# Kernel optimization log

Hardware: AMD Instinct MI355X
Metric: run time of the kernel (lower is better)

## Reference

```python
import jax, jax.numpy as jnp
import numpy as np

T, B, IN_DIM, D_VALUE, D_KEY = 1024, 8, 512, 64, 64
EPS = 1e-8

def setup_inputs() -> dict:
    key = jax.random.key(0)
    ks = jax.random.split(key, 7)
    s = 1.0 / np.sqrt(IN_DIM)
    return {
        "x":  jax.random.normal(ks[0], (T, B, IN_DIM), dtype=jnp.float32),
        "Wv": jax.random.uniform(ks[1], (D_VALUE, IN_DIM), jnp.float32, -s, s),
        "bv": jax.random.uniform(ks[2], (D_VALUE,), jnp.float32, -s, s),
        "Wk": jax.random.uniform(ks[3], (D_KEY, IN_DIM), jnp.float32, -s, s),
        "bk": jax.random.uniform(ks[4], (D_KEY,), jnp.float32, -s, s),
        "Wa": jax.random.uniform(ks[5], (D_KEY, IN_DIM), jnp.float32, -s, s),
        "ba": jax.random.uniform(ks[6], (D_KEY,), jnp.float32, -s, s),
    }

def reference(x, Wv, bv, Wk, bk, Wa, ba):
    # Projections: x (T,B,in_dim) -> v (T,B,d), k (T,B,n), alpha (T,B,n)
    v = jnp.einsum('tbi,di->tbd', x, Wv) + bv
    k = jnp.einsum('tbi,ni->tbn', x, Wk) + bk
    alpha = jax.nn.sigmoid(jnp.einsum('tbi,ni->tbn', x, Wa) + ba)
    # outer product per timestep: (T,B,d,n)
    outer = jnp.einsum('tbd,tbn->tbdn', v, k)
    # log-space cumulative decay, normalized by final cumprod
    log_cumprod = jnp.cumsum(jnp.log(jnp.maximum(alpha, EPS)), axis=0)  # (T,B,n)
    cumprod = jnp.exp(log_cumprod)
    decay = cumprod / (cumprod[-1:] + EPS)
    weighted = outer * decay[:, :, None, :]  # (T,B,d,n)
    S = jnp.cumsum(weighted, axis=0)
    return S
```

## Files before the change

### kernel.cpp

```cpp
#include <hip/hip_runtime.h>
#include <math.h>

#define T_DIM  1024
#define B_DIM  8
#define IN_D   512
#define NROWS  (T_DIM * B_DIM)
#define EPSF   1e-8f

#define CHUNK  16
#define NCHUNK (T_DIM / CHUNK)
#define SEG    16
#define NSEG   (T_DIM / SEG)

typedef float vfloat4 __attribute__((ext_vector_type(4)));

#define OFF_WT   0
#define OFF_V    (OFF_WT + IN_D * 192)
#define OFF_K    (OFF_V  + NROWS * 64)
#define OFF_Z    (OFF_K  + NROWS * 64)
#define OFF_SEG  (OFF_Z  + NROWS * 64)
#define OFF_TOT  (OFF_SEG + NSEG * B_DIM * 64)
#define OFF_P    (OFF_TOT + B_DIM * 64)

__global__ void k0_wt(const float* __restrict__ Wv, const float* __restrict__ Wk,
                      const float* __restrict__ Wa, float* __restrict__ Wt) {
    int idx = blockIdx.x * 256 + threadIdx.x;
    int i = idx / 192, c = idx % 192;
    float v;
    if (c < 64)       v = Wv[c * IN_D + i];
    else if (c < 128) v = Wk[(c - 64) * IN_D + i];
    else              v = Wa[(c - 128) * IN_D + i];
    Wt[i * 192 + c] = v;
}

__global__ __launch_bounds__(256) void k1_proj(
        const float* __restrict__ x, const float* __restrict__ Wt,
        const float* __restrict__ bv, const float* __restrict__ bk, const float* __restrict__ ba,
        float* __restrict__ V, float* __restrict__ Kb, float* __restrict__ Zb) {
    __shared__ float xs[2][32][32];
    __shared__ float wsm[2][32][192];
    const int tid  = threadIdx.x;
    const int h    = tid >> 7;
    const int t7   = tid & 127;
    const int rq   = t7 >> 4;
    const int cq   = t7 & 15;
    const int row0 = blockIdx.x * 32;

    float4 acc[4][3];
#pragma unroll
    for (int j = 0; j < 4; ++j)
#pragma unroll
        for (int m = 0; m < 3; ++m) acc[j][m] = make_float4(0.f, 0.f, 0.f, 0.f);

    for (int s = 0; s < 8; ++s) {
#pragma unroll
        for (int q = 0; q < 2; ++q) {
            int idx = tid + q * 256;
            int hh = idx >> 8, r = idx & 31, f = (idx >> 5) & 7;
            float4 v4 = reinterpret_cast<const float4*>(x)[((row0 + r) * IN_D + hh * 256 + s * 32 + f * 4) >> 2];
            xs[hh][f * 4 + 0][r] = v4.x;
            xs[hh][f * 4 + 1][r] = v4.y;
            xs[hh][f * 4 + 2][r] = v4.z;
            xs[hh][f * 4 + 3][r] = v4.w;
        }
#pragma unroll
        for (int q = 0; q < 12; ++q) {
            int idx = tid + q * 256;
            int hh = idx / 1536;
            int rem = idx - hh * 1536;
            int kk = rem / 48;
            int f  = rem - kk * 48;
            float4 v4 = reinterpret_cast<const float4*>(Wt)[((hh * 256 + s * 32 + kk) * 192 + f * 4) >> 2];
            *reinterpret_cast<float4*>(&wsm[hh][kk][f * 4]) = v4;
        }
        __syncthreads();

#pragma unroll 4
        for (int kk = 0; kk < 32; ++kk) {
            float4 xv = *reinterpret_cast<const float4*>(&xs[h][kk][rq * 4]);
#pragma unroll
            for (int m = 0; m < 3; ++m) {
                float4 wq = *reinterpret_cast<const float4*>(&wsm[h][kk][m * 64 + cq * 4]);
#pragma unroll
                for (int j = 0; j < 4; ++j) {
                    float xx = (&xv.x)[j];
                    acc[j][m].x = fmaf(xx, wq.x, acc[j][m].x);
                    acc[j][m].y = fmaf(xx, wq.y, acc[j][m].y);
                    acc[j][m].z = fmaf(xx, wq.z, acc[j][m].z);
                    acc[j][m].w = fmaf(xx, wq.w, acc[j][m].w);
                }
            }
        }
        __syncthreads();
    }

    float* red = &wsm[0][0][0];
    if (h == 1) {
#pragma unroll
        for (int j = 0; j < 4; ++j)
#pragma unroll
            for (int m = 0; m < 3; ++m)
                *reinterpret_cast<float4*>(&red[t7 * 52 + (j * 3 + m) * 4]) = acc[j][m];
    }
    __syncthreads();
    if (h == 0) {
        float4 bv4 = *reinterpret_cast<const float4*>(&bv[cq * 4]);
        float4 bk4 = *reinterpret_cast<const float4*>(&bk[cq * 4]);
        float4 ba4 = *reinterpret_cast<const float4*>(&ba[cq * 4]);
#pragma unroll
        for (int j = 0; j < 4; ++j) {
            int row = row0 + rq * 4 + j;
#pragma unroll
            for (int m = 0; m < 3; ++m) {
                float4 o = *reinterpret_cast<const float4*>(&red[t7 * 52 + (j * 3 + m) * 4]);
                o.x += (&acc[j][m].x)[0];
                o.x = acc[j][m].x + (&o.x)[0] - acc[j][m].x;
            }
            float4 o0 = *reinterpret_cast<const float4*>(&red[t7 * 52 + (j * 3 + 0) * 4]);
            float4 o1 = *reinterpret_cast<const float4*>(&red[t7 * 52 + (j * 3 + 1) * 4]);
            float4 o2 = *reinterpret_cast<const float4*>(&red[t7 * 52 + (j * 3 + 2) * 4]);
            float4 r0, r1, r2;
            r0.x = acc[j][0].x + o0.x + bv4.x; r0.y = acc[j][0].y + o0.y + bv4.y;
            r0.z = acc[j][0].z + o0.z + bv4.z; r0.w = acc[j][0].w + o0.w + bv4.w;
            r1.x = acc[j][1].x + o1.x + bk4.x; r1.y = acc[j][1].y + o1.y + bk4.y;
            r1.z = acc[j][1].z + o1.z + bk4.z; r1.w = acc[j][1].w + o1.w + bk4.w;
            r2.x = acc[j][2].x + o2.x + ba4.x; r2.y = acc[j][2].y + o2.y + ba4.y;
            r2.z = acc[j][2].z + o2.z + ba4.z; r2.w = acc[j][2].w + o2.w + ba4.w;
            *reinterpret_cast<float4*>(&V [row * 64 + cq * 4]) = r0;
            *reinterpret_cast<float4*>(&Kb[row * 64 + cq * 4]) = r1;
            *reinterpret_cast<float4*>(&Zb[row * 64 + cq * 4]) = r2;
        }
    }
}

__global__ void k2a_logs(float* __restrict__ Z, float* __restrict__ seg) {
    int b = blockIdx.x & 7, s = blockIdx.x >> 3;
    int n = threadIdx.x;
    int base = b * 64 + n;
    float accv = 0.f;
#pragma unroll
    for (int i = 0; i < SEG; ++i) {
        int t = s * SEG + i;
        float z = Z[t * 512 + base];
        float a = 1.f / (1.f + expf(-z));
        float l = logf(fmaxf(a, EPSF));
        Z[t * 512 + base] = l;
        accv += l;
    }
    seg[s * 512 + base] = accv;
}

__global__ void k2b_scan(float* __restrict__ seg, float* __restrict__ tot) {
    int i = threadIdx.x;
    float vals[NSEG];
#pragma unroll
    for (int s = 0; s < NSEG; ++s) vals[s] = seg[s * 512 + i];
    float run = 0.f;
#pragma unroll
    for (int s = 0; s < NSEG; ++s) { seg[s * 512 + i] = run; run += vals[s]; }
    tot[i] = run;
}

__global__ void k2c_w(const float* __restrict__ Z, const float* __restrict__ seg,
                      const float* __restrict__ tot, float* __restrict__ Kb) {
    int b = blockIdx.x & 7, s = blockIdx.x >> 3;
    int n = threadIdx.x;
    int base = b * 64 + n;
    float run = seg[s * 512 + base];
    float invden = 1.f / (expf(tot[base]) + EPSF);
#pragma unroll
    for (int i = 0; i < SEG; ++i) {
        int t = s * SEG + i;
        run += Z[t * 512 + base];
        Kb[t * 512 + base] *= expf(run) * invden;
    }
}

__global__ __launch_bounds__(256) void k3_partial(const float* __restrict__ V,
                                                  const float* __restrict__ W,
                                                  float* __restrict__ P) {
    __shared__ float vs[CHUNK * 64];
    __shared__ float wsh[CHUNK * 64];
    int b = blockIdx.x & 7, cch = blockIdx.x >> 3;
    int tid = threadIdx.x;
    int dg = tid >> 4, n4 = tid & 15;
    {
        int il = tid >> 4, f = tid & 15;
        int row = (cch * CHUNK + il) * 8 + b;
        reinterpret_cast<float4*>(vs)[il * 16 + f]  = reinterpret_cast<const float4*>(V)[row * 16 + f];
        reinterpret_cast<float4*>(wsh)[il * 16 + f] = reinterpret_cast<const float4*>(W)[row * 16 + f];
    }
    __syncthreads();
    float4 acc[4];
#pragma unroll
    for (int q = 0; q < 4; ++q) acc[q] = make_float4(0.f, 0.f, 0.f, 0.f);

#pragma unroll
    for (int i = 0; i < CHUNK; ++i) {
        float4 wv = reinterpret_cast<const float4*>(wsh)[i * 16 + n4];
#pragma unroll
        for (int q = 0; q < 4; ++q) {
            float vd = vs[i * 64 + dg + 16 * q];
            acc[q].x = fmaf(vd, wv.x, acc[q].x);
            acc[q].y = fmaf(vd, wv.y, acc[q].y);
            acc[q].z = fmaf(vd, wv.z, acc[q].z);
            acc[q].w = fmaf(vd, wv.w, acc[q].w);
        }
    }
    float* Pp = P + (cch * 8 + b) * 4096;
#pragma unroll
    for (int q = 0; q < 4; ++q)
        *reinterpret_cast<float4*>(Pp + (dg + 16 * q) * 64 + 4 * n4) = acc[q];
}

__global__ __launch_bounds__(256) void k4_prefix(float* __restrict__ P) {
    int gid = blockIdx.x * 256 + threadIdx.x;
    int b = gid >> 12, dn = gid & 4095;
    float run = 0.f;
#pragma unroll
    for (int c = 0; c < NCHUNK; ++c) {
        float v = P[(c * 8 + b) * 4096 + dn];
        P[(c * 8 + b) * 4096 + dn] = run;
        run += v;
    }
}

__global__ __launch_bounds__(256) void k5_main(const float* __restrict__ V,
                                               const float* __restrict__ W,
                                               const float* __restrict__ P,
                                               float* __restrict__ S) {
    __shared__ float vs[CHUNK * 64];
    __shared__ float wsh[CHUNK * 64];
    int b = blockIdx.x & 7, cch = blockIdx.x >> 3;
    int tid = threadIdx.x;
    int dg = tid >> 4, n4 = tid & 15;
    {
        int il = tid >> 4, f = tid & 15;
        int row = (cch * CHUNK + il) * 8 + b;
        reinterpret_cast<float4*>(vs)[il * 16 + f]  = reinterpret_cast<const float4*>(V)[row * 16 + f];
        reinterpret_cast<float4*>(wsh)[il * 16 + f] = reinterpret_cast<const float4*>(W)[row * 16 + f];
    }
    vfloat4 acc[4];
    const float* Pp = P + (cch * 8 + b) * 4096;
#pragma unroll
    for (int q = 0; q < 4; ++q)
        acc[q] = *reinterpret_cast<const vfloat4*>(Pp + (dg + 16 * q) * 64 + 4 * n4);
    __syncthreads();

#pragma unroll
    for (int i = 0; i < CHUNK; ++i) {
        float4 wv = reinterpret_cast<const float4*>(wsh)[i * 16 + n4];
        int t = cch * CHUNK + i;
        float* Sb = S + (size_t)t * 32768 + b * 4096;
#pragma unroll
        for (int q = 0; q < 4; ++q) {
            float vd = vs[i * 64 + dg + 16 * q];
            acc[q].x = fmaf(vd, wv.x, acc[q].x);
            acc[q].y = fmaf(vd, wv.y, acc[q].y);
            acc[q].z = fmaf(vd, wv.z, acc[q].z);
            acc[q].w = fmaf(vd, wv.w, acc[q].w);
            __builtin_nontemporal_store(acc[q],
                reinterpret_cast<vfloat4*>(Sb + (dg + 16 * q) * 64 + 4 * n4));
        }
    }
}

extern "C" void kernel_launch(void* const* d_in, const int* in_sizes, int n_in,
                              void* d_out, int out_size, void* d_ws, size_t ws_size,
                              hipStream_t stream) {
    const float* x  = (const float*)d_in[0];
    const float* Wv = (const float*)d_in[1];
    const float* bv = (const float*)d_in[2];
    const float* Wk = (const float*)d_in[3];
    const float* bk = (const float*)d_in[4];
    const float* Wa = (const float*)d_in[5];
    const float* ba = (const float*)d_in[6];
    float* S  = (float*)d_out;
    float* ws = (float*)d_ws;

    float* Wt  = ws + OFF_WT;
    float* V   = ws + OFF_V;
    float* Kb  = ws + OFF_K;
    float* Zb  = ws + OFF_Z;
    float* seg = ws + OFF_SEG;
    float* tot = ws + OFF_TOT;
    float* P   = ws + OFF_P;

    k0_wt     <<<384, 256, 0, stream>>>(Wv, Wk, Wa, Wt);
    k1_proj   <<<256, 256, 0, stream>>>(x, Wt, bv, bk, ba, V, Kb, Zb);
    k2a_logs  <<<512,  64, 0, stream>>>(Zb, seg);
    k2b_scan  <<<  1, 512, 0, stream>>>(seg, tot);
    k2c_w     <<<512,  64, 0, stream>>>(Zb, seg, tot, Kb);
    k3_partial<<<512, 256, 0, stream>>>(V, Kb, P);
    k4_prefix <<<128, 256, 0, stream>>>(P);
    k5_main   <<<512, 256, 0, stream>>>(V, Kb, P, S);
}
```

Baseline: 212.7 us.

## Fuse log-sigmoid scan into single wave-shuffle kernel and drop weight transpose

```diff
diff --git a/kernel.cpp b/kernel.cpp
--- a/kernel.cpp
+++ b/kernel.cpp
@@ -9,32 +9,17 @@
 
 #define CHUNK  16
 #define NCHUNK (T_DIM / CHUNK)
-#define SEG    16
-#define NSEG   (T_DIM / SEG)
 
 typedef float vfloat4 __attribute__((ext_vector_type(4)));
 
-#define OFF_WT   0
-#define OFF_V    (OFF_WT + IN_D * 192)
+#define OFF_V    0
 #define OFF_K    (OFF_V  + NROWS * 64)
 #define OFF_Z    (OFF_K  + NROWS * 64)
-#define OFF_SEG  (OFF_Z  + NROWS * 64)
-#define OFF_TOT  (OFF_SEG + NSEG * B_DIM * 64)
-#define OFF_P    (OFF_TOT + B_DIM * 64)
-
-__global__ void k0_wt(const float* __restrict__ Wv, const float* __restrict__ Wk,
-                      const float* __restrict__ Wa, float* __restrict__ Wt) {
-    int idx = blockIdx.x * 256 + threadIdx.x;
-    int i = idx / 192, c = idx % 192;
-    float v;
-    if (c < 64)       v = Wv[c * IN_D + i];
-    else if (c < 128) v = Wk[(c - 64) * IN_D + i];
-    else              v = Wa[(c - 128) * IN_D + i];
-    Wt[i * 192 + c] = v;
-}
-
-__global__ __launch_bounds__(256) void k1_proj(
-        const float* __restrict__ x, const float* __restrict__ Wt,
+#define OFF_P    (OFF_Z  + NROWS * 64)
+
+__global__ __launch_bounds__(256) void kA_proj(
+        const float* __restrict__ x,
+        const float* __restrict__ Wv, const float* __restrict__ Wk, const float* __restrict__ Wa,
         const float* __restrict__ bv, const float* __restrict__ bk, const float* __restrict__ ba,
         float* __restrict__ V, float* __restrict__ Kb, float* __restrict__ Zb) {
     __shared__ float xs[2][32][32];
@@ -66,12 +51,16 @@
 #pragma unroll
         for (int q = 0; q < 12; ++q) {
             int idx = tid + q * 256;
-            int hh = idx / 1536;
-            int rem = idx - hh * 1536;
-            int kk = rem / 48;
-            int f  = rem - kk * 48;
-            float4 v4 = reinterpret_cast<const float4*>(Wt)[((hh * 256 + s * 32 + kk) * 192 + f * 4) >> 2];
-            *reinterpret_cast<float4*>(&wsm[hh][kk][f * 4]) = v4;
+            int c = idx % 192;
+            int rest = idx / 192;
+            int hh = rest >> 3, fq = rest & 7;
+            const float* Wsrc = (c < 64) ? Wv : ((c < 128) ? Wk : Wa);
+            int ci = (c < 64) ? c : ((c < 128) ? c - 64 : c - 128);
+            float4 v4 = *reinterpret_cast<const float4*>(Wsrc + ci * IN_D + hh * 256 + s * 32 + fq * 4);
+            wsm[hh][fq * 4 + 0][c] = v4.x;
+            wsm[hh][fq * 4 + 1][c] = v4.y;
+            wsm[hh][fq * 4 + 2][c] = v4.z;
+            wsm[hh][fq * 4 + 3][c] = v4.w;
         }
         __syncthreads();
 
@@ -110,12 +99,6 @@
 #pragma unroll
         for (int j = 0; j < 4; ++j) {
             int row = row0 + rq * 4 + j;
-#pragma unroll
-            for (int m = 0; m < 3; ++m) {
-                float4 o = *reinterpret_cast<const float4*>(&red[t7 * 52 + (j * 3 + m) * 4]);
-                o.x += (&acc[j][m].x)[0];
-                o.x = acc[j][m].x + (&o.x)[0] - acc[j][m].x;
-            }
             float4 o0 = *reinterpret_cast<const float4*>(&red[t7 * 52 + (j * 3 + 0) * 4]);
             float4 o1 = *reinterpret_cast<const float4*>(&red[t7 * 52 + (j * 3 + 1) * 4]);
             float4 o2 = *reinterpret_cast<const float4*>(&red[t7 * 52 + (j * 3 + 2) * 4]);
@@ -133,50 +116,38 @@
     }
 }
 
-__global__ void k2a_logs(float* __restrict__ Z, float* __restrict__ seg) {
-    int b = blockIdx.x & 7, s = blockIdx.x >> 3;
-    int n = threadIdx.x;
-    int base = b * 64 + n;
-    float accv = 0.f;
-#pragma unroll
-    for (int i = 0; i < SEG; ++i) {
-        int t = s * SEG + i;
-        float z = Z[t * 512 + base];
-        float a = 1.f / (1.f + expf(-z));
-        float l = logf(fmaxf(a, EPSF));
-        Z[t * 512 + base] = l;
-        accv += l;
-    }
-    seg[s * 512 + base] = accv;
-}
-
-__global__ void k2b_scan(float* __restrict__ seg, float* __restrict__ tot) {
-    int i = threadIdx.x;
-    float vals[NSEG];
-#pragma unroll
-    for (int s = 0; s < NSEG; ++s) vals[s] = seg[s * 512 + i];
-    float run = 0.f;
-#pragma unroll
-    for (int s = 0; s < NSEG; ++s) { seg[s * 512 + i] = run; run += vals[s]; }
-    tot[i] = run;
-}
-
-__global__ void k2c_w(const float* __restrict__ Z, const float* __restrict__ seg,
-                      const float* __restrict__ tot, float* __restrict__ Kb) {
-    int b = blockIdx.x & 7, s = blockIdx.x >> 3;
-    int n = threadIdx.x;
-    int base = b * 64 + n;
-    float run = seg[s * 512 + base];
-    float invden = 1.f / (expf(tot[base]) + EPSF);
-#pragma unroll
-    for (int i = 0; i < SEG; ++i) {
-        int t = s * SEG + i;
-        run += Z[t * 512 + base];
-        Kb[t * 512 + base] *= expf(run) * invden;
-    }
-}
-
-__global__ __launch_bounds__(256) void k3_partial(const float* __restrict__ V,
+__global__ __launch_bounds__(64) void kB_scan(const float* __restrict__ Z,
+                                              float* __restrict__ Kb) {
+    const int ch   = blockIdx.x;
+    const int lane = threadIdx.x;
+    const int t0   = lane * 16;
+    float run[16];
+    float acc = 0.f;
+#pragma unroll
+    for (int i = 0; i < 16; ++i) {
+        float z = Z[(t0 + i) * 512 + ch];
+        float l = fminf(z, 0.f) - __logf(1.f + __expf(-fabsf(z)));
+        l = fmaxf(l, -18.4206807f);
+        acc += l;
+        run[i] = acc;
+    }
+    float incl = acc;
+#pragma unroll
+    for (int d = 1; d < 64; d <<= 1) {
+        float tmp = __shfl_up(incl, d, 64);
+        incl += (lane >= d) ? tmp : 0.f;
+    }
+    float excl = incl - acc;
+    float Ltot = __shfl(incl, 63, 64);
+    float inv  = 1.f / (__expf(Ltot) + EPSF);
+#pragma unroll
+    for (int i = 0; i < 16; ++i) {
+        int idx = (t0 + i) * 512 + ch;
+        Kb[idx] *= __expf(excl + run[i]) * inv;
+    }
+}
+
+__global__ __launch_bounds__(256) void kC_partial(const float* __restrict__ V,
                                                   const float* __restrict__ W,
                                                   float* __restrict__ P) {
     __shared__ float vs[CHUNK * 64];
@@ -213,19 +184,18 @@
         *reinterpret_cast<float4*>(Pp + (dg + 16 * q) * 64 + 4 * n4) = acc[q];
 }
 
-__global__ __launch_bounds__(256) void k4_prefix(float* __restrict__ P) {
+__global__ __launch_bounds__(256) void kD_prefix(float* __restrict__ P) {
     int gid = blockIdx.x * 256 + threadIdx.x;
     int b = gid >> 12, dn = gid & 4095;
+    float vals[NCHUNK];
+#pragma unroll
+    for (int c = 0; c < NCHUNK; ++c) vals[c] = P[(c * 8 + b) * 4096 + dn];
     float run = 0.f;
 #pragma unroll
-    for (int c = 0; c < NCHUNK; ++c) {
-        float v = P[(c * 8 + b) * 4096 + dn];
-        P[(c * 8 + b) * 4096 + dn] = run;
-        run += v;
-    }
-}
-
-__global__ __launch_bounds__(256) void k5_main(const float* __restrict__ V,
+    for (int c = 0; c < NCHUNK; ++c) { P[(c * 8 + b) * 4096 + dn] = run; run += vals[c]; }
+}
+
+__global__ __launch_bounds__(256) void kE_main(const float* __restrict__ V,
                                                const float* __restrict__ W,
                                                const float* __restrict__ P,
                                                float* __restrict__ S) {
@@ -278,20 +248,14 @@
     float* S  = (float*)d_out;
     float* ws = (float*)d_ws;
 
-    float* Wt  = ws + OFF_WT;
     float* V   = ws + OFF_V;
     float* Kb  = ws + OFF_K;
     float* Zb  = ws + OFF_Z;
-    float* seg = ws + OFF_SEG;
-    float* tot = ws + OFF_TOT;
     float* P   = ws + OFF_P;
 
-    k0_wt     <<<384, 256, 0, stream>>>(Wv, Wk, Wa, Wt);
-    k1_proj   <<<256, 256, 0, stream>>>(x, Wt, bv, bk, ba, V, Kb, Zb);
-    k2a_logs  <<<512,  64, 0, stream>>>(Zb, seg);
-    k2b_scan  <<<  1, 512, 0, stream>>>(seg, tot);
-    k2c_w     <<<512,  64, 0, stream>>>(Zb, seg, tot, Kb);
-    k3_partial<<<512, 256, 0, stream>>>(V, Kb, P);
-    k4_prefix <<<128, 256, 0, stream>>>(P);
-    k5_main   <<<512, 256, 0, stream>>>(V, Kb, P, S);
-}
+    kA_proj   <<<256, 256, 0, stream>>>(x, Wv, Wk, Wa, bv, bk, ba, V, Kb, Zb);
+    kB_scan   <<<512,  64, 0, stream>>>(Zb, Kb);
+    kC_partial<<<512, 256, 0, stream>>>(V, Kb, P);
+    kD_prefix <<<128, 256, 0, stream>>>(P);
+    kE_main   <<<512, 256, 0, stream>>>(V, Kb, P, S);
+}
```

Measured after the change: 221.3 us. 4.0% more time.
